# Optimization experiments

Hardware: AMD Instinct MI355X
Metric: run time of the kernel (lower is better)

## Reference

```python
import jax, jax.numpy as jnp
import numpy as np

N = 100000   # nodes
E = 1000000  # edges
D = 64       # in_features
D_OUT = 64   # out_features


def setup_inputs() -> dict:
    key = jax.random.key(0)
    k1, k2, k3, k4, k5, k6 = jax.random.split(key, 6)
    h = jax.random.normal(k1, (N, D), dtype=jnp.float32)          # current node features ndata['h']
    i = jax.random.normal(k2, (N, D), dtype=jnp.float32)          # initial features ndata['i']
    edge_src = jax.random.randint(k3, (E,), 0, N, dtype=jnp.int32)
    edge_dst = jax.random.randint(k4, (E,), 0, N, dtype=jnp.int32)
    edge_w = jax.random.uniform(k5, (E,), dtype=jnp.float32)      # scalar edge weight edata['x']
    stdv = 1.0 / np.sqrt(D_OUT)
    weight = jax.random.uniform(k6, (2 * D, D_OUT), dtype=jnp.float32,
                                minval=-stdv, maxval=stdv)        # variant=True -> in = 2*D
    return {
        "h": h, "i": i, "weight": weight, "edge_w": edge_w,
        "lamda": jnp.float32(0.5), "alpha": jnp.float32(0.1),
        "edge_src": edge_src, "edge_dst": edge_dst, "layer_idx": 4,
    }


def reference(h, i, weight, edge_w, lamda, alpha, edge_src, edge_dst, layer_idx):
    # theta = min(1, log(lamda/layer_idx + 1))
    theta = jnp.minimum(jnp.float32(1.0), jnp.log(lamda / layer_idx + 1.0))
    # update_all(u_mul_e('h','x','m'), sum('m','h')): edge-weighted gather-scatter SpMM
    m = h[edge_src] * edge_w[:, None]                 # [E, D]
    h_agg = jax.ops.segment_sum(m, edge_dst, num_segments=h.shape[0])  # [N, D]
    # variant=True branch
    support = jnp.concatenate([h_agg, i], axis=1)     # [N, 2D]
    r = (1.0 - alpha) * h_agg + alpha * i             # [N, D]
    out = theta * (support @ weight) + (1.0 - theta) * r
    # residual=True
    out = out + i
    return out
```

## Files before the change

kernel.cpp:

```cpp
#include <hip/hip_runtime.h>
#include <math.h>


#define DFEAT 64
#define BINSZ 128
#define NBINS 1024
#define CAP   2048
#define CHUNK 4096
#define TPB   512
#define ASTR  72

typedef unsigned long long u64;
typedef __attribute__((ext_vector_type(8))) short bf16x8;
typedef __attribute__((ext_vector_type(4))) float f32x4;

__device__ inline unsigned short to_bf16(float f) {
    unsigned u = __float_as_uint(f);
    u += 0x7FFF + ((u >> 16) & 1);
    return (unsigned short)(u >> 16);
}
__device__ inline float bf_up(unsigned short s) {
    return __uint_as_float(((unsigned)s) << 16);
}

__global__ __launch_bounds__(512) void bin_fill_kernel(
    const float* __restrict__ h, const float* __restrict__ weight,
    const int* __restrict__ e_src, const int* __restrict__ e_dst,
    const float* __restrict__ e_w, int* __restrict__ gcur,
    u64* __restrict__ bucket, ushort* __restrict__ h16,
    ushort* __restrict__ w16, int E, int total4) {
    __shared__ u64 staging[CHUNK];
    __shared__ unsigned short binOf[CHUNK];
    __shared__ int hist[NBINS], offs[NBINS], gbase[NBINS], cur[NBINS];
    __shared__ int part[TPB];

    int tid = threadIdx.x;
    int gid = blockIdx.x * TPB + tid;
    int nthreads = gridDim.x * TPB;

    for (int i = gid; i < total4; i += nthreads) {
        float4 v = ((const float4*)h)[i];
        ushort4 o;
        o.x = to_bf16(v.x); o.y = to_bf16(v.y);
        o.z = to_bf16(v.z); o.w = to_bf16(v.w);
        ((ushort4*)h16)[i] = o;
    }
    if (gid < 8192) {
        int j = gid & 7, l = (gid >> 3) & 63, cs = gid >> 9;
        int c = cs >> 2, s = cs & 3, q = l >> 4, m = l & 15;
        w16[gid] = to_bf16(weight[(s * 32 + q * 8 + j) * DFEAT + c * 16 + m]);
    }

    int e0 = blockIdx.x * CHUNK;
    int cc = min(CHUNK, E - e0);

    hist[tid] = 0; hist[tid + 512] = 0;
    __syncthreads();

    int d[8], s[8];
    float w[8];
#pragma unroll
    for (int j = 0; j < 8; ++j) {
        int e = e0 + j * TPB + tid;
        if (e < E) { d[j] = e_dst[e]; s[j] = e_src[e]; w[j] = e_w[e]; }
        else d[j] = -1;
    }
#pragma unroll
    for (int j = 0; j < 8; ++j)
        if (d[j] >= 0) atomicAdd(&hist[d[j] >> 7], 1);
    __syncthreads();

    int a = hist[2 * tid], b = hist[2 * tid + 1];
    part[tid] = a + b;
    __syncthreads();
    for (int ofs = 1; ofs < TPB; ofs <<= 1) {
        int t = (tid >= ofs) ? part[tid - ofs] : 0;
        __syncthreads();
        part[tid] += t;
        __syncthreads();
    }
    int excl = part[tid] - (a + b);
    offs[2 * tid] = excl;         cur[2 * tid] = excl;
    offs[2 * tid + 1] = excl + a; cur[2 * tid + 1] = excl + a;
    __syncthreads();

#pragma unroll
    for (int j = 0; j < 8; ++j) {
        if (d[j] >= 0) {
            int bb = d[j] >> 7;
            int p = atomicAdd(&cur[bb], 1);
            unsigned lo = (unsigned)s[j] | ((unsigned)(d[j] & 127) << 24);
            staging[p] = ((u64)(unsigned)__float_as_int(w[j]) << 32) | lo;
            binOf[p] = (unsigned short)bb;
        }
    }
    __syncthreads();

    for (int t = tid; t < NBINS; t += TPB) {
        int c = hist[t];
        gbase[t] = (c > 0) ? atomicAdd(&gcur[t], c) : 0;
    }
    __syncthreads();

#pragma unroll
    for (int j = 0; j < 8; ++j) {
        int p = j * TPB + tid;
        if (p < cc) {
            int bb = binOf[p];
            bucket[(size_t)bb * CAP + gbase[bb] + (p - offs[bb])] = staging[p];
        }
    }
}

__global__ __launch_bounds__(512) void spmm_kernel(
    const ushort* __restrict__ h16, const u64* __restrict__ bucket,
    const int* __restrict__ gcur, const ushort* __restrict__ w16,
    const float* __restrict__ ifeat,
    const float* __restrict__ lamda_p, const float* __restrict__ alpha_p,
    const int* __restrict__ layer_p,
    float* __restrict__ out, int N) {
    __shared__ u64 sorted[CAP];
    __shared__ __align__(16) ushort agg16[BINSZ * ASTR];
    __shared__ int hist[BINSZ], start[BINSZ], cur[BINSZ], part[BINSZ];

    int tid = threadIdx.x;
    int bin = blockIdx.x;
    int base = bin << 7;
    int cnt = gcur[bin];
    const u64* bk = bucket + (size_t)bin * CAP;

    if (tid < BINSZ) hist[tid] = 0;
    __syncthreads();

    for (int p = tid; p < cnt; p += TPB)
        atomicAdd(&hist[(((unsigned)bk[p]) >> 24) & 127], 1);
    __syncthreads();

    int v = 0;
    if (tid < BINSZ) { v = hist[tid]; part[tid] = v; }
    __syncthreads();
    for (int ofs = 1; ofs < BINSZ; ofs <<= 1) {
        int t = (tid < BINSZ && tid >= ofs) ? part[tid - ofs] : 0;
        __syncthreads();
        if (tid < BINSZ) part[tid] += t;
        __syncthreads();
    }
    if (tid < BINSZ) { start[tid] = part[tid] - v; cur[tid] = part[tid] - v; }
    __syncthreads();

    for (int p = tid; p < cnt; p += TPB) {
        u64 e = bk[p];
        int pos = atomicAdd(&cur[(((unsigned)e) >> 24) & 127], 1);
        sorted[pos] = e;
    }
    __syncthreads();

    int lane = tid & 63, wv = tid >> 6;
    int g = lane >> 4, m = lane & 15;
    int nn = min(BINSZ, N - base);

    for (int k = 0; k < 16; ++k) {
        int nl = wv * 16 + k;
        if (nl >= nn) break;
        int d = hist[nl];
        int b0 = start[nl];
        float a0 = 0.f, a1 = 0.f, a2 = 0.f, a3 = 0.f;
        for (int t0 = 0; t0 < d; t0 += 16) {
#pragma unroll
            for (int s = 0; s < 4; ++s) {
                int idx = t0 + s * 4 + g;
                u64 e = sorted[b0 + min(idx, d - 1)];
                float wt = (idx < d) ? __int_as_float((int)(e >> 32)) : 0.f;
                int src = ((unsigned)e) & 0xFFFFFF;
                ushort4 hv = *(const ushort4*)(h16 + (size_t)src * DFEAT + m * 4);
                a0 += wt * bf_up(hv.x);
                a1 += wt * bf_up(hv.y);
                a2 += wt * bf_up(hv.z);
                a3 += wt * bf_up(hv.w);
            }
        }
        a0 += __shfl_xor(a0, 16); a1 += __shfl_xor(a1, 16);
        a2 += __shfl_xor(a2, 16); a3 += __shfl_xor(a3, 16);
        a0 += __shfl_xor(a0, 32); a1 += __shfl_xor(a1, 32);
        a2 += __shfl_xor(a2, 32); a3 += __shfl_xor(a3, 32);
        if (g == 0) {
            ushort4 o;
            o.x = to_bf16(a0); o.y = to_bf16(a1);
            o.z = to_bf16(a2); o.w = to_bf16(a3);
            *(ushort4*)(agg16 + nl * ASTR + m * 4) = o;
        }
    }

    float alf = alpha_p[0];
    float theta = fminf(1.0f, logf(lamda_p[0] / (float)layer_p[0] + 1.0f));
    int q = lane >> 4;

    bf16x8 faA[2], faI[2];
#pragma unroll
    for (int s = 0; s < 2; ++s)
        faA[s] = *(const bf16x8*)(agg16 + (wv * 16 + m) * ASTR + s * 32 + q * 8);
    {
        const float* ip = ifeat + (size_t)min(base + wv * 16 + m, N - 1) * DFEAT;
#pragma unroll
        for (int s = 0; s < 2; ++s) {
            float4 v0 = *(const float4*)(ip + s * 32 + q * 8);
            float4 v1 = *(const float4*)(ip + s * 32 + q * 8 + 4);
            bf16x8 t;
            t[0] = (short)to_bf16(v0.x); t[1] = (short)to_bf16(v0.y);
            t[2] = (short)to_bf16(v0.z); t[3] = (short)to_bf16(v0.w);
            t[4] = (short)to_bf16(v1.x); t[5] = (short)to_bf16(v1.y);
            t[6] = (short)to_bf16(v1.z); t[7] = (short)to_bf16(v1.w);
            faI[s] = t;
        }
    }

    f32x4 acc[4] = {{0.f, 0.f, 0.f, 0.f}, {0.f, 0.f, 0.f, 0.f},
                    {0.f, 0.f, 0.f, 0.f}, {0.f, 0.f, 0.f, 0.f}};
#pragma unroll
    for (int c = 0; c < 4; ++c) {
#pragma unroll
        for (int s = 0; s < 2; ++s) {
            bf16x8 bA = *(const bf16x8*)(w16 + ((c * 4 + s) * 64 + lane) * 8);
            acc[c] = __builtin_amdgcn_mfma_f32_16x16x32_bf16(faA[s], bA, acc[c], 0, 0, 0);
            bf16x8 bI = *(const bf16x8*)(w16 + ((c * 4 + s + 2) * 64 + lane) * 8);
            acc[c] = __builtin_amdgcn_mfma_f32_16x16x32_bf16(faI[s], bI, acc[c], 0, 0, 0);
        }
    }

#pragma unroll
    for (int c = 0; c < 4; ++c) {
        int col = c * 16 + m;
#pragma unroll
        for (int r = 0; r < 4; ++r) {
            int rowL = wv * 16 + q * 4 + r;
            int row = base + rowL;
            if (row < N) {
                float av = bf_up(agg16[rowL * ASTR + col]);
                float iv = ifeat[(size_t)row * DFEAT + col];
                out[(size_t)row * DFEAT + col] =
                    theta * acc[c][r] +
                    (1.f - theta) * ((1.f - alf) * av + alf * iv) + iv;
            }
        }
    }
}

extern "C" void kernel_launch(void* const* d_in, const int* in_sizes, int n_in,
                              void* d_out, int out_size, void* d_ws, size_t ws_size,
                              hipStream_t stream) {
    const float* h       = (const float*)d_in[0];
    const float* ifeat   = (const float*)d_in[1];
    const float* weight  = (const float*)d_in[2];
    const float* edge_w  = (const float*)d_in[3];
    const float* lamda_p = (const float*)d_in[4];
    const float* alpha_p = (const float*)d_in[5];
    const int*   e_src   = (const int*)d_in[6];
    const int*   e_dst   = (const int*)d_in[7];
    const int*   layer_p = (const int*)d_in[8];
    float* out = (float*)d_out;

    int N = in_sizes[0] / DFEAT;
    int E = in_sizes[3];
    int nbins = (N + BINSZ - 1) >> 7;

    int* gcur = (int*)d_ws;
    u64* bucket = (u64*)((char*)d_ws + 4096);
    ushort* h16 = (ushort*)((char*)bucket + (size_t)NBINS * CAP * sizeof(u64));
    ushort* w16 = h16 + (size_t)N * DFEAT;

    hipMemsetAsync(gcur, 0, NBINS * sizeof(int), stream);

    int total4 = N * DFEAT / 4;
    bin_fill_kernel<<<(E + CHUNK - 1) / CHUNK, TPB, 0, stream>>>(
        h, weight, e_src, e_dst, edge_w, gcur, bucket, h16, w16, E, total4);

    spmm_kernel<<<nbins, TPB, 0, stream>>>(
        h16, bucket, gcur, w16, ifeat, lamda_p, alpha_p, layer_p, out, N);
}
```

Baseline: 162.4 us.

## Compute per-node degrees in bin fill and skip per-bin histogram pass

The binning kernel now also counts each node's in-degree with global atomics into a workspace array that is zeroed by the existing memset. The SpMM kernel reads these degrees instead of re-reading the bucket to build a local histogram, so one pass over bucket memory and its shared atomics go away. The scatter loop now loads bucket entries into registers first, and the gather loop predicates out padded lanes instead of clamping. The cost is one million extra global atomics, contended on random nodes, in the first kernel plus a larger memset.

```diff
diff --git a/kernel.cpp b/kernel.cpp
--- a/kernel.cpp
+++ b/kernel.cpp
@@ -27,8 +27,8 @@
     const float* __restrict__ h, const float* __restrict__ weight,
     const int* __restrict__ e_src, const int* __restrict__ e_dst,
     const float* __restrict__ e_w, int* __restrict__ gcur,
-    u64* __restrict__ bucket, ushort* __restrict__ h16,
-    ushort* __restrict__ w16, int E, int total4) {
+    int* __restrict__ deg, u64* __restrict__ bucket,
+    ushort* __restrict__ h16, ushort* __restrict__ w16, int E, int total4) {
     __shared__ u64 staging[CHUNK];
     __shared__ unsigned short binOf[CHUNK];
     __shared__ int hist[NBINS], offs[NBINS], gbase[NBINS], cur[NBINS];
@@ -67,7 +67,10 @@
     }
 #pragma unroll
     for (int j = 0; j < 8; ++j)
-        if (d[j] >= 0) atomicAdd(&hist[d[j] >> 7], 1);
+        if (d[j] >= 0) {
+            atomicAdd(&hist[d[j] >> 7], 1);
+            atomicAdd(&deg[d[j]], 1);
+        }
     __syncthreads();
 
     int a = hist[2 * tid], b = hist[2 * tid + 1];
@@ -114,14 +117,14 @@
 
 __global__ __launch_bounds__(512) void spmm_kernel(
     const ushort* __restrict__ h16, const u64* __restrict__ bucket,
-    const int* __restrict__ gcur, const ushort* __restrict__ w16,
-    const float* __restrict__ ifeat,
+    const int* __restrict__ gcur, const int* __restrict__ deg,
+    const ushort* __restrict__ w16, const float* __restrict__ ifeat,
     const float* __restrict__ lamda_p, const float* __restrict__ alpha_p,
     const int* __restrict__ layer_p,
     float* __restrict__ out, int N) {
     __shared__ u64 sorted[CAP];
     __shared__ __align__(16) ushort agg16[BINSZ * ASTR];
-    __shared__ int hist[BINSZ], start[BINSZ], cur[BINSZ], part[BINSZ];
+    __shared__ int dsh[BINSZ], start[BINSZ], cur[BINSZ], part[BINSZ];
 
     int tid = threadIdx.x;
     int bin = blockIdx.x;
@@ -129,15 +132,11 @@
     int cnt = gcur[bin];
     const u64* bk = bucket + (size_t)bin * CAP;
 
-    if (tid < BINSZ) hist[tid] = 0;
-    __syncthreads();
-
-    for (int p = tid; p < cnt; p += TPB)
-        atomicAdd(&hist[(((unsigned)bk[p]) >> 24) & 127], 1);
-    __syncthreads();
-
     int v = 0;
-    if (tid < BINSZ) { v = hist[tid]; part[tid] = v; }
+    if (tid < BINSZ) {
+        v = (base + tid < N) ? deg[base + tid] : 0;
+        dsh[tid] = v; part[tid] = v;
+    }
     __syncthreads();
     for (int ofs = 1; ofs < BINSZ; ofs <<= 1) {
         int t = (tid < BINSZ && tid >= ofs) ? part[tid - ofs] : 0;
@@ -148,10 +147,18 @@
     if (tid < BINSZ) { start[tid] = part[tid] - v; cur[tid] = part[tid] - v; }
     __syncthreads();
 
-    for (int p = tid; p < cnt; p += TPB) {
-        u64 e = bk[p];
-        int pos = atomicAdd(&cur[(((unsigned)e) >> 24) & 127], 1);
-        sorted[pos] = e;
+    {
+        u64 e[4]; int pp[4], np = 0;
+#pragma unroll
+        for (int j = 0; j < 4; ++j) {
+            int p = tid + j * TPB;
+            if (p < cnt) { e[np] = bk[p]; pp[np] = p; ++np; }
+        }
+        for (int j = 0; j < np; ++j) {
+            int pos = atomicAdd(&cur[(((unsigned)e[j]) >> 24) & 127], 1);
+            sorted[pos] = e[j];
+        }
+        (void)pp;
     }
     __syncthreads();
 
@@ -159,24 +166,26 @@
     int g = lane >> 4, m = lane & 15;
     int nn = min(BINSZ, N - base);
 
-    for (int k = 0; k < 16; ++k) {
+    int kmax = min(16, nn - wv * 16);
+    for (int k = 0; k < kmax; ++k) {
         int nl = wv * 16 + k;
-        if (nl >= nn) break;
-        int d = hist[nl];
+        int d = dsh[nl];
         int b0 = start[nl];
         float a0 = 0.f, a1 = 0.f, a2 = 0.f, a3 = 0.f;
         for (int t0 = 0; t0 < d; t0 += 16) {
 #pragma unroll
             for (int s = 0; s < 4; ++s) {
                 int idx = t0 + s * 4 + g;
-                u64 e = sorted[b0 + min(idx, d - 1)];
-                float wt = (idx < d) ? __int_as_float((int)(e >> 32)) : 0.f;
-                int src = ((unsigned)e) & 0xFFFFFF;
-                ushort4 hv = *(const ushort4*)(h16 + (size_t)src * DFEAT + m * 4);
-                a0 += wt * bf_up(hv.x);
-                a1 += wt * bf_up(hv.y);
-                a2 += wt * bf_up(hv.z);
-                a3 += wt * bf_up(hv.w);
+                if (idx < d) {
+                    u64 e = sorted[b0 + idx];
+                    float wt = __int_as_float((int)(e >> 32));
+                    int src = ((unsigned)e) & 0xFFFFFF;
+                    ushort4 hv = *(const ushort4*)(h16 + (size_t)src * DFEAT + m * 4);
+                    a0 += wt * bf_up(hv.x);
+                    a1 += wt * bf_up(hv.y);
+                    a2 += wt * bf_up(hv.z);
+                    a3 += wt * bf_up(hv.w);
+                }
             }
         }
         a0 += __shfl_xor(a0, 16); a1 += __shfl_xor(a1, 16);
@@ -264,16 +273,19 @@
     int nbins = (N + BINSZ - 1) >> 7;
 
     int* gcur = (int*)d_ws;
-    u64* bucket = (u64*)((char*)d_ws + 4096);
+    int* deg = gcur + NBINS;
+    size_t degbytes = (size_t)(NBINS + N) * sizeof(int);
+    size_t bucket_off = (degbytes + 4095) & ~(size_t)4095;
+    u64* bucket = (u64*)((char*)d_ws + bucket_off);
     ushort* h16 = (ushort*)((char*)bucket + (size_t)NBINS * CAP * sizeof(u64));
     ushort* w16 = h16 + (size_t)N * DFEAT;
 
-    hipMemsetAsync(gcur, 0, NBINS * sizeof(int), stream);
+    hipMemsetAsync(gcur, 0, degbytes, stream);
 
     int total4 = N * DFEAT / 4;
     bin_fill_kernel<<<(E + CHUNK - 1) / CHUNK, TPB, 0, stream>>>(
-        h, weight, e_src, e_dst, edge_w, gcur, bucket, h16, w16, E, total4);
+        h, weight, e_src, e_dst, edge_w, gcur, deg, bucket, h16, w16, E, total4);
 
     spmm_kernel<<<nbins, TPB, 0, stream>>>(
-        h16, bucket, gcur, w16, ifeat, lamda_p, alpha_p, layer_p, out, N);
-}
+        h16, bucket, gcur, deg, w16, ifeat, lamda_p, alpha_p, layer_p, out, N);
+}
```

Result: slower. 201.0 us (+23.8%).

## Replace shared-memory barrier scans with wave shuffles and single-pass bin sort

Applied to the files above, without the earlier changes.

Both kernels replace the block-wide Hillis-Steele prefix scans, which needed about twenty __syncthreads each, with wave-level __shfl_up scans plus a small cross-wave fixup. The spmm kernel now loads each bucket's edges into registers once. It records the atomic rank taken during the histogram and scatters straight into the sorted array, dropping the second atomic pass and the second global read. The gather loop now skips padded lanes with a branch instead of doing a clamped dummy load. This cuts barrier and redundant-load overhead, but the register arrays are sized for 4 edges per thread, so a bin holding more than 2048 entries (the CAP limit) would overflow.

```diff
diff --git a/kernel.cpp b/kernel.cpp
--- a/kernel.cpp
+++ b/kernel.cpp
@@ -32,11 +32,12 @@
     __shared__ u64 staging[CHUNK];
     __shared__ unsigned short binOf[CHUNK];
     __shared__ int hist[NBINS], offs[NBINS], gbase[NBINS], cur[NBINS];
-    __shared__ int part[TPB];
+    __shared__ int wsum[8];
 
     int tid = threadIdx.x;
     int gid = blockIdx.x * TPB + tid;
     int nthreads = gridDim.x * TPB;
+    int lane = tid & 63, wv = tid >> 6;
 
     for (int i = gid; i < total4; i += nthreads) {
         float4 v = ((const float4*)h)[i];
@@ -71,15 +72,22 @@
     __syncthreads();
 
     int a = hist[2 * tid], b = hist[2 * tid + 1];
-    part[tid] = a + b;
-    __syncthreads();
-    for (int ofs = 1; ofs < TPB; ofs <<= 1) {
-        int t = (tid >= ofs) ? part[tid - ofs] : 0;
-        __syncthreads();
-        part[tid] += t;
-        __syncthreads();
-    }
-    int excl = part[tid] - (a + b);
+    int x = a + b;
+    int xs = x;
+#pragma unroll
+    for (int o = 1; o < 64; o <<= 1) {
+        int t = __shfl_up(xs, o);
+        if (lane >= o) xs += t;
+    }
+    if (lane == 63) wsum[wv] = xs;
+    __syncthreads();
+    if (tid == 0) {
+        int r = 0;
+#pragma unroll
+        for (int i = 0; i < 8; ++i) { int t = wsum[i]; wsum[i] = r; r += t; }
+    }
+    __syncthreads();
+    int excl = xs - x + wsum[wv];
     offs[2 * tid] = excl;         cur[2 * tid] = excl;
     offs[2 * tid + 1] = excl + a; cur[2 * tid + 1] = excl + a;
     __syncthreads();
@@ -121,7 +129,8 @@
     float* __restrict__ out, int N) {
     __shared__ u64 sorted[CAP];
     __shared__ __align__(16) ushort agg16[BINSZ * ASTR];
-    __shared__ int hist[BINSZ], start[BINSZ], cur[BINSZ], part[BINSZ];
+    __shared__ int hist[BINSZ], start[BINSZ];
+    __shared__ int wsum2;
 
     int tid = threadIdx.x;
     int bin = blockIdx.x;
@@ -129,39 +138,49 @@
     int cnt = gcur[bin];
     const u64* bk = bucket + (size_t)bin * CAP;
 
+    u64 e[4]; int np = 0;
+#pragma unroll
+    for (int j = 0; j < 4; ++j) {
+        int p = tid + j * TPB;
+        if (p < cnt) { e[np] = bk[p]; ++np; }
+    }
+
     if (tid < BINSZ) hist[tid] = 0;
     __syncthreads();
 
-    for (int p = tid; p < cnt; p += TPB)
-        atomicAdd(&hist[(((unsigned)bk[p]) >> 24) & 127], 1);
-    __syncthreads();
-
-    int v = 0;
-    if (tid < BINSZ) { v = hist[tid]; part[tid] = v; }
-    __syncthreads();
-    for (int ofs = 1; ofs < BINSZ; ofs <<= 1) {
-        int t = (tid < BINSZ && tid >= ofs) ? part[tid - ofs] : 0;
-        __syncthreads();
-        if (tid < BINSZ) part[tid] += t;
-        __syncthreads();
-    }
-    if (tid < BINSZ) { start[tid] = part[tid] - v; cur[tid] = part[tid] - v; }
-    __syncthreads();
-
-    for (int p = tid; p < cnt; p += TPB) {
-        u64 e = bk[p];
-        int pos = atomicAdd(&cur[(((unsigned)e) >> 24) & 127], 1);
-        sorted[pos] = e;
+    int rk[4], dl[4];
+    for (int j = 0; j < np; ++j) {
+        dl[j] = (((unsigned)e[j]) >> 24) & 127;
+        rk[j] = atomicAdd(&hist[dl[j]], 1);
     }
     __syncthreads();
 
     int lane = tid & 63, wv = tid >> 6;
+    if (tid < BINSZ) {
+        int v = hist[tid];
+        int xs = v;
+#pragma unroll
+        for (int o = 1; o < 64; o <<= 1) {
+            int t = __shfl_up(xs, o);
+            if (lane >= o) xs += t;
+        }
+        if (tid == 63) wsum2 = xs;
+        start[tid] = xs - v;
+    }
+    __syncthreads();
+    if (tid >= 64 && tid < BINSZ) start[tid] += wsum2;
+    __syncthreads();
+
+    for (int j = 0; j < np; ++j)
+        sorted[start[dl[j]] + rk[j]] = e[j];
+    __syncthreads();
+
     int g = lane >> 4, m = lane & 15;
     int nn = min(BINSZ, N - base);
 
-    for (int k = 0; k < 16; ++k) {
+    int kmax = min(16, nn - wv * 16);
+    for (int k = 0; k < kmax; ++k) {
         int nl = wv * 16 + k;
-        if (nl >= nn) break;
         int d = hist[nl];
         int b0 = start[nl];
         float a0 = 0.f, a1 = 0.f, a2 = 0.f, a3 = 0.f;
@@ -169,14 +188,16 @@
 #pragma unroll
             for (int s = 0; s < 4; ++s) {
                 int idx = t0 + s * 4 + g;
-                u64 e = sorted[b0 + min(idx, d - 1)];
-                float wt = (idx < d) ? __int_as_float((int)(e >> 32)) : 0.f;
-                int src = ((unsigned)e) & 0xFFFFFF;
-                ushort4 hv = *(const ushort4*)(h16 + (size_t)src * DFEAT + m * 4);
-                a0 += wt * bf_up(hv.x);
-                a1 += wt * bf_up(hv.y);
-                a2 += wt * bf_up(hv.z);
-                a3 += wt * bf_up(hv.w);
+                if (idx < d) {
+                    u64 ee = sorted[b0 + idx];
+                    float wt = __int_as_float((int)(ee >> 32));
+                    int src = ((unsigned)ee) & 0xFFFFFF;
+                    ushort4 hv = *(const ushort4*)(h16 + (size_t)src * DFEAT + m * 4);
+                    a0 += wt * bf_up(hv.x);
+                    a1 += wt * bf_up(hv.y);
+                    a2 += wt * bf_up(hv.z);
+                    a3 += wt * bf_up(hv.w);
+                }
             }
         }
         a0 += __shfl_xor(a0, 16); a1 += __shfl_xor(a1, 16);
```

Result: no change. 164.7 us (+1.5%).
